# Optimization experiments

Hardware: AMD Instinct MI355X
Metric: run time of the kernel (lower is better)

The kernel has to match this reference:

```python
import jax, jax.numpy as jnp
import numpy as np

LN_EPS = 1e-5

def setup_inputs() -> dict:
    key = jax.random.key(0)
    ks = jax.random.split(key, 4)
    B, T, N, D, G = 8, 48, 1024, 64, 256
    x = jax.random.normal(ks[0], (B, T, N, D), dtype=jnp.float32)
    view = jax.random.uniform(ks[1], (G, N), dtype=jnp.float32)
    w = jax.random.normal(ks[2], (N, D, D), dtype=jnp.float32) * 0.02
    b = jax.random.normal(ks[3], (1, N, D), dtype=jnp.float32) * 0.02
    gamma = jnp.ones((D,), dtype=jnp.float32)
    beta = jnp.zeros((D,), dtype=jnp.float32)
    return {"x": x, "view": view, "w": w, "b": b, "gamma": gamma, "beta": beta}

def _layernorm(x, gamma, beta):
    mu = jnp.mean(x, axis=-1, keepdims=True)
    var = jnp.mean(jnp.square(x - mu), axis=-1, keepdims=True)
    return (x - mu) * jax.lax.rsqrt(var + LN_EPS) * gamma + beta

def reference(x, view, w, b, gamma, beta):
    # per-node linear transform: [B,T,N,D] x [N,D,D] -> [B,T,N,D]
    h = jnp.einsum('btni,nio->btno', x, w)
    h = h + b[0]  # bias broadcast over batch and time
    # grid aggregation via view mapping: [B,T,N,D] x [G,N] -> [B,T,G,D]
    g = jnp.einsum('btnd,gn->btgd', h, view)
    return _layernorm(g, gamma, beta)
```

## Files before the change

### kernel.cpp

```cpp
#include <hip/hip_runtime.h>
#include <stdint.h>
#include <stddef.h>


#define LNEPS 1e-5f

typedef __attribute__((ext_vector_type(8))) short bf16x8;
typedef __attribute__((ext_vector_type(4))) float f32x4;
typedef union { unsigned u[4]; bf16x8 v; } fragu;

static __device__ __forceinline__ unsigned rne(unsigned u) {
    return u + 0x7FFFu + ((u >> 16) & 1u);
}
static __device__ __forceinline__ void split_pair(float a, float b,
                                                  unsigned& hw_, unsigned& lw_) {
    unsigned ra = rne(__float_as_uint(a));
    unsigned rb = rne(__float_as_uint(b));
    hw_ = (ra >> 16) | (rb & 0xFFFF0000u);
    float fa = a - __uint_as_float(ra & 0xFFFF0000u);
    float fb = b - __uint_as_float(rb & 0xFFFF0000u);
    unsigned sa = rne(__float_as_uint(fa));
    unsigned sb = rne(__float_as_uint(fb));
    lw_ = (sa >> 16) | (sb & 0xFFFF0000u);
}
static __device__ __forceinline__ unsigned packhl(float vv) {
    unsigned r = rne(__float_as_uint(vv));
    unsigned hif = r & 0xFFFF0000u;
    float res = vv - __uint_as_float(hif);
    unsigned s = rne(__float_as_uint(res));
    return hif | (s >> 16);
}

static __device__ __forceinline__ void gll16(const void* g, void* l) {
    __builtin_amdgcn_global_load_lds(
        (const __attribute__((address_space(1))) void*)g,
        (__attribute__((address_space(3))) void*)l, 16, 0, 0);
}

#define WS_H   0u
#define WS_VH  100663296u
#define WS_VL  101187584u
#define WS_VB  101711872u

__global__ __launch_bounds__(256) void k0_prep(
        const float* __restrict__ view, const float* __restrict__ bias,
        unsigned short* __restrict__ vh, unsigned short* __restrict__ vl,
        float* __restrict__ vb) {
    const int g = blockIdx.x;
    const int tid = threadIdx.x;
    float4 vv = *(const float4*)(view + g * 1024 + tid * 4);
    unsigned h01, l01, h23, l23;
    split_pair(vv.x, vv.y, h01, l01);
    split_pair(vv.z, vv.w, h23, l23);
    *(uint2*)(vh + g * 1024 + tid * 4) = make_uint2(h01, h23);
    *(uint2*)(vl + g * 1024 + tid * 4) = make_uint2(l01, l23);
    const int q = tid >> 6, d = tid & 63;
    const float* vrow = view + g * 1024;
    float a = 0.f;
    #pragma unroll 8
    for (int nn = q * 256; nn < q * 256 + 256; ++nn)
        a = fmaf(vrow[nn], bias[nn * 64 + d], a);
    __shared__ float red[4][64];
    red[q][d] = a;
    __syncthreads();
    if (tid < 64)
        vb[g * 64 + tid] = red[0][tid] + red[1][tid] + red[2][tid] + red[3][tid];
}

__global__ __launch_bounds__(1024, 4) void k1_node(
        const float* __restrict__ x, const float* __restrict__ w,
        unsigned char* __restrict__ hb) {
    __shared__ float xs[16 * 16 * 64];
    __shared__ unsigned T[16 * 16 * 68];
    const int tid = threadIdx.x;
    const int l  = tid & 63, wv = tid >> 6;
    const int lc = l & 15,  lg = l >> 4;
    const int ng = blockIdx.x & 63, btg = blockIdx.x >> 6;
    const int n0 = ng * 16;
    const int bt_base = btg * 96;
    const int n = n0 + wv;

    bf16x8 bh[4][2], bl[4][2];
    #pragma unroll
    for (int cs = 0; cs < 4; ++cs) {
        #pragma unroll
        for (int kc = 0; kc < 2; ++kc) {
            const float* wp = w + (size_t)n * 4096 + (size_t)(kc * 32 + lg * 8) * 64
                                + cs * 16 + lc;
            float e[8];
            #pragma unroll
            for (int j = 0; j < 8; ++j) e[j] = wp[(size_t)j * 64];
            fragu H, L;
            #pragma unroll
            for (int k2 = 0; k2 < 4; ++k2)
                split_pair(e[2 * k2], e[2 * k2 + 1], H.u[k2], L.u[k2]);
            bh[cs][kc] = H.v;
            bl[cs][kc] = L.v;
        }
    }

#define K1_STAGE(T_) do {                                                     \
    _Pragma("unroll")                                                         \
    for (int c_ = 0; c_ < 4; ++c_) {                                          \
        int u_ = c_ * 1024 + tid;                                             \
        int btl_ = u_ >> 8, r_ = u_ & 255;                                    \
        int nn_ = r_ >> 4, q_ = r_ & 15;                                      \
        int ibp_ = q_ >> 1, hf_ = q_ & 1;                                     \
        int ibg_ = ibp_ ^ (btl_ & 7);                                         \
        const unsigned char* src_ = (const unsigned char*)x                   \
            + (size_t)(bt_base + (T_) * 16 + btl_) * 262144u                  \
            + (size_t)(n0 + nn_) * 256u + ibg_ * 32 + hf_ * 16;               \
        gll16(src_, (unsigned char*)xs + c_ * 16384 + wv * 1024);             \
    }                                                                         \
} while (0)

    K1_STAGE(0);
    for (int t = 0; t < 6; ++t) {
        __syncthreads();
        float4 xq[4];
        #pragma unroll
        for (int kc = 0; kc < 2; ++kc) {
            int ibp = (kc * 4 + lg) ^ (lc & 7);
            const float* rp = xs + lc * 1024 + wv * 64 + ibp * 8;
            xq[kc * 2]     = *(const float4*)(rp);
            xq[kc * 2 + 1] = *(const float4*)(rp + 4);
        }
        __syncthreads();
        if (t < 5) K1_STAGE(t + 1);

        bf16x8 ah[2], al[2];
        #pragma unroll
        for (int kc = 0; kc < 2; ++kc) {
            fragu H, L;
            split_pair(xq[kc * 2].x,     xq[kc * 2].y,     H.u[0], L.u[0]);
            split_pair(xq[kc * 2].z,     xq[kc * 2].w,     H.u[1], L.u[1]);
            split_pair(xq[kc * 2 + 1].x, xq[kc * 2 + 1].y, H.u[2], L.u[2]);
            split_pair(xq[kc * 2 + 1].z, xq[kc * 2 + 1].w, H.u[3], L.u[3]);
            ah[kc] = H.v;
            al[kc] = L.v;
        }
        f32x4 acc[4];
        #pragma unroll
        for (int cs = 0; cs < 4; ++cs) acc[cs] = (f32x4){0.f, 0.f, 0.f, 0.f};
        #pragma unroll
        for (int cs = 0; cs < 4; ++cs) {
            #pragma unroll
            for (int kc = 0; kc < 2; ++kc) {
                acc[cs] = __builtin_amdgcn_mfma_f32_16x16x32_bf16(ah[kc], bh[cs][kc], acc[cs], 0, 0, 0);
                acc[cs] = __builtin_amdgcn_mfma_f32_16x16x32_bf16(ah[kc], bl[cs][kc], acc[cs], 0, 0, 0);
                acc[cs] = __builtin_amdgcn_mfma_f32_16x16x32_bf16(al[kc], bh[cs][kc], acc[cs], 0, 0, 0);
                acc[cs] = __builtin_amdgcn_mfma_f32_16x16x32_bf16(al[kc], bl[cs][kc], acc[cs], 0, 0, 0);
            }
        }
        #pragma unroll
        for (int cs = 0; cs < 4; ++cs) {
            #pragma unroll
            for (int j = 0; j < 4; ++j)
                T[wv * 1088 + (lg * 4 + j) * 68 + cs * 16 + lc] = packhl(acc[cs][j]);
        }
        __syncthreads();
        {
            int btl = tid >> 6, d = tid & 63;
            unsigned vv[16];
            #pragma unroll
            for (int nn = 0; nn < 16; ++nn) vv[nn] = T[nn * 1088 + btl * 68 + d];
            unsigned hd[8], ld[8];
            #pragma unroll
            for (int k = 0; k < 8; ++k) {
                hd[k] = (vv[2 * k] >> 16) | (vv[2 * k + 1] & 0xFFFF0000u);
                ld[k] = (vv[2 * k] & 0xFFFFu) | (vv[2 * k + 1] << 16);
            }
            unsigned char* dst = hb + (size_t)(bt_base + t * 16 + btl) * 262144u
                                    + (size_t)d * 4096u + ng * 64;
            ((uint4*)dst)[0] = make_uint4(hd[0], hd[1], hd[2], hd[3]);
            ((uint4*)dst)[1] = make_uint4(hd[4], hd[5], hd[6], hd[7]);
            ((uint4*)dst)[2] = make_uint4(ld[0], ld[1], ld[2], ld[3]);
            ((uint4*)dst)[3] = make_uint4(ld[4], ld[5], ld[6], ld[7]);
        }
    }
#undef K1_STAGE
}

#define KB2 24576

__global__ __launch_bounds__(256, 3) void k2_grid(
        const unsigned short* __restrict__ vh, const unsigned short* __restrict__ vl,
        const unsigned char* __restrict__ hb, const float* __restrict__ vb,
        const float* __restrict__ gamma, const float* __restrict__ beta,
        float* __restrict__ out) {
    __shared__ __align__(16) unsigned char smem[2 * KB2];
    const int tid = threadIdx.x;
    const int l  = tid & 63;
    const int wv = tid >> 6;
    const int b  = blockIdx.x;
    const int bm = (b >> 3) & 1;
    const int bt = (b & 7) + (b >> 4) * 8;
    const int lc = l & 15, lg = l >> 4;

    const unsigned short* a_src[4];
    int a_dst[4];
    #pragma unroll
    for (int c = 0; c < 4; ++c) {
        int id = (wv * 4 + c) * 64 + l;
        int row = id >> 3;
        int slot = id & 7;
        int sg = slot ^ (row & 7);
        int plg = sg >> 2, kcg = sg & 3;
        const unsigned short* pl = plg ? vl : vh;
        a_src[c] = pl + (size_t)(bm * 128 + row) * 1024 + kcg * 8;
        a_dst[c] = (wv * 4 + c) * 1024;
    }
    const unsigned char* b_src[2];
    int b_dst[2];
    #pragma unroll
    for (int c = 0; c < 2; ++c) {
        int id = (wv * 2 + c) * 64 + l;
        int d_ = id >> 3;
        int slot = id & 7;
        int sg = slot ^ (d_ & 7);
        b_src[c] = hb + (size_t)bt * 262144u + (size_t)d_ * 4096u
                      + (sg >> 2) * 64 + ((sg >> 1) & 1) * 32 + (sg & 1) * 16;
        b_dst[c] = 16384 + (wv * 2 + c) * 1024;
    }
    int aoff[2][2];
    #pragma unroll
    for (int st = 0; st < 2; ++st)
        #pragma unroll
        for (int pl = 0; pl < 2; ++pl) {
            int row = wv * 32 + st * 16 + lc;
            aoff[st][pl] = row * 128 + ((((pl << 2) | lg) ^ (row & 7)) * 16);
        }
    int boff[4][2];
    #pragma unroll
    for (int cs = 0; cs < 4; ++cs)
        #pragma unroll
        for (int pl = 0; pl < 2; ++pl) {
            int d_ = cs * 16 + lc;
            int sg = ((lg >> 1) << 2) | (pl << 1) | (lg & 1);
            boff[cs][pl] = 16384 + d_ * 128 + ((sg ^ (d_ & 7)) * 16);
        }

    f32x4 acc[2][4];
    #pragma unroll
    for (int st = 0; st < 2; ++st)
        #pragma unroll
        for (int cs = 0; cs < 4; ++cs)
            acc[st][cs] = (f32x4){0.f, 0.f, 0.f, 0.f};

#define K2_STAGE(KB, S) do {                                                  \
    _Pragma("unroll")                                                         \
    for (int c_ = 0; c_ < 4; ++c_)                                            \
        gll16(a_src[c_] + (size_t)(S) * 32, smem + (KB) + a_dst[c_]);         \
    _Pragma("unroll")                                                         \
    for (int c_ = 0; c_ < 2; ++c_)                                            \
        gll16(b_src[c_] + (size_t)(S) * 128, smem + (KB) + b_dst[c_]);        \
} while (0)

    K2_STAGE(0, 0);
    __syncthreads();
    int kb = 0;
    for (int s = 0; s < 32; ++s) {
        if (s + 1 < 32) K2_STAGE(kb ^ KB2, s + 1);
        bf16x8 a0h = *(const bf16x8*)(smem + kb + aoff[0][0]);
        bf16x8 a0l = *(const bf16x8*)(smem + kb + aoff[0][1]);
        bf16x8 a1h = *(const bf16x8*)(smem + kb + aoff[1][0]);
        bf16x8 a1l = *(const bf16x8*)(smem + kb + aoff[1][1]);
        #pragma unroll
        for (int cs = 0; cs < 4; ++cs) {
            bf16x8 bhf = *(const bf16x8*)(smem + kb + boff[cs][0]);
            bf16x8 blf = *(const bf16x8*)(smem + kb + boff[cs][1]);
            acc[0][cs] = __builtin_amdgcn_mfma_f32_16x16x32_bf16(a0h, bhf, acc[0][cs], 0, 0, 0);
            acc[0][cs] = __builtin_amdgcn_mfma_f32_16x16x32_bf16(a0h, blf, acc[0][cs], 0, 0, 0);
            acc[0][cs] = __builtin_amdgcn_mfma_f32_16x16x32_bf16(a0l, bhf, acc[0][cs], 0, 0, 0);
            acc[1][cs] = __builtin_amdgcn_mfma_f32_16x16x32_bf16(a1h, bhf, acc[1][cs], 0, 0, 0);
            acc[1][cs] = __builtin_amdgcn_mfma_f32_16x16x32_bf16(a1h, blf, acc[1][cs], 0, 0, 0);
            acc[1][cs] = __builtin_amdgcn_mfma_f32_16x16x32_bf16(a1l, bhf, acc[1][cs], 0, 0, 0);
        }
        __syncthreads();
        kb ^= KB2;
    }

    float gam[4], bet[4];
    #pragma unroll
    for (int cs = 0; cs < 4; ++cs) {
        gam[cs] = gamma[cs * 16 + lc];
        bet[cs] = beta[cs * 16 + lc];
    }
    #pragma unroll
    for (int st = 0; st < 2; ++st) {
        #pragma unroll
        for (int j = 0; j < 4; ++j) {
            int g = bm * 128 + wv * 32 + st * 16 + lg * 4 + j;
            float v[4];
            float s1 = 0.f, s2 = 0.f;
            #pragma unroll
            for (int cs = 0; cs < 4; ++cs) {
                v[cs] = acc[st][cs][j] + vb[g * 64 + cs * 16 + lc];
                s1 += v[cs];
                s2 += v[cs] * v[cs];
            }
            s1 += __shfl_xor(s1, 1);  s2 += __shfl_xor(s2, 1);
            s1 += __shfl_xor(s1, 2);  s2 += __shfl_xor(s2, 2);
            s1 += __shfl_xor(s1, 4);  s2 += __shfl_xor(s2, 4);
            s1 += __shfl_xor(s1, 8);  s2 += __shfl_xor(s2, 8);
            float mu  = s1 * 0.015625f;
            float var = s2 * 0.015625f - mu * mu;
            float inv = rsqrtf(var + LNEPS);
            size_t ob = (size_t)bt * 16384u + (size_t)g * 64u;
            #pragma unroll
            for (int cs = 0; cs < 4; ++cs)
                out[ob + cs * 16 + lc] = (v[cs] - mu) * inv * gam[cs] + bet[cs];
        }
    }
#undef K2_STAGE
}

extern "C" void kernel_launch(void* const* d_in, const int* in_sizes, int n_in,
                              void* d_out, int out_size, void* d_ws, size_t ws_size,
                              hipStream_t stream) {
    (void)in_sizes; (void)n_in; (void)out_size; (void)ws_size;
    const float* x     = (const float*)d_in[0];
    const float* view  = (const float*)d_in[1];
    const float* w     = (const float*)d_in[2];
    const float* bias  = (const float*)d_in[3];
    const float* gamma = (const float*)d_in[4];
    const float* beta  = (const float*)d_in[5];
    float* out = (float*)d_out;

    char* ws = (char*)d_ws;
    unsigned char* hb  = (unsigned char*)(ws + WS_H);
    unsigned short* vh = (unsigned short*)(ws + WS_VH);
    unsigned short* vl = (unsigned short*)(ws + WS_VL);
    float* vb          = (float*)(ws + WS_VB);

    hipLaunchKernelGGL(k0_prep, dim3(256), dim3(256), 0, stream,
                       view, bias, vh, vl, vb);
    hipLaunchKernelGGL(k1_node, dim3(256), dim3(1024), 0, stream, x, w, hb);
    hipLaunchKernelGGL(k2_grid, dim3(768), dim3(256), 0, stream,
                       vh, vl, hb, vb, gamma, beta, out);
}
```

Baseline: 270.1 us.

## Load x directly into registers in k1 and use fine-grained waitcnt barriers in k2

In the node-transform kernel, the LDS staging of x through async global-to-LDS loads and its double barrier are removed. Each wave now reads its x fragments straight from global memory into registers, which frees the xs shared buffer and drops the minimum-blocks launch bound. In the grid kernel, __syncthreads is replaced by an explicit s_waitcnt vmcnt(6) plus s_barrier, so the prefetch of the next stage can stay in flight while the current stage is consumed. This trades the previous load overlap in k1 for less LDS traffic and synchronisation, and it relies on hand-counted outstanding-load counts being correct.

```diff
diff --git a/kernel.cpp b/kernel.cpp
--- a/kernel.cpp
+++ b/kernel.cpp
@@ -67,17 +67,15 @@
         vb[g * 64 + tid] = red[0][tid] + red[1][tid] + red[2][tid] + red[3][tid];
 }
 
-__global__ __launch_bounds__(1024, 4) void k1_node(
+__global__ __launch_bounds__(1024) void k1_node(
         const float* __restrict__ x, const float* __restrict__ w,
         unsigned char* __restrict__ hb) {
-    __shared__ float xs[16 * 16 * 64];
     __shared__ unsigned T[16 * 16 * 68];
     const int tid = threadIdx.x;
     const int l  = tid & 63, wv = tid >> 6;
     const int lc = l & 15,  lg = l >> 4;
     const int ng = blockIdx.x & 63, btg = blockIdx.x >> 6;
-    const int n0 = ng * 16;
-    const int bt_base = btg * 96;
+    const int n0 = ng * 16, bt_base = btg * 96;
     const int n = n0 + wv;
 
     bf16x8 bh[4][2], bl[4][2];
@@ -99,46 +97,35 @@
         }
     }
 
-#define K1_STAGE(T_) do {                                                     \
-    _Pragma("unroll")                                                         \
-    for (int c_ = 0; c_ < 4; ++c_) {                                          \
-        int u_ = c_ * 1024 + tid;                                             \
-        int btl_ = u_ >> 8, r_ = u_ & 255;                                    \
-        int nn_ = r_ >> 4, q_ = r_ & 15;                                      \
-        int ibp_ = q_ >> 1, hf_ = q_ & 1;                                     \
-        int ibg_ = ibp_ ^ (btl_ & 7);                                         \
-        const unsigned char* src_ = (const unsigned char*)x                   \
-            + (size_t)(bt_base + (T_) * 16 + btl_) * 262144u                  \
-            + (size_t)(n0 + nn_) * 256u + ibg_ * 32 + hf_ * 16;               \
-        gll16(src_, (unsigned char*)xs + c_ * 16384 + wv * 1024);             \
-    }                                                                         \
-} while (0)
-
-    K1_STAGE(0);
+    const int btl = tid >> 6;
+    const int dT  = tid & 63;
+
     for (int t = 0; t < 6; ++t) {
-        __syncthreads();
-        float4 xq[4];
-        #pragma unroll
-        for (int kc = 0; kc < 2; ++kc) {
-            int ibp = (kc * 4 + lg) ^ (lc & 7);
-            const float* rp = xs + lc * 1024 + wv * 64 + ibp * 8;
-            xq[kc * 2]     = *(const float4*)(rp);
-            xq[kc * 2 + 1] = *(const float4*)(rp + 4);
-        }
-        __syncthreads();
-        if (t < 5) K1_STAGE(t + 1);
+        const float* xp = x + (size_t)(bt_base + t * 16 + lc) * 65536u
+                            + (size_t)n * 64 + lg * 8;
+        float4 x0 = *(const float4*)(xp);
+        float4 x1 = *(const float4*)(xp + 4);
+        float4 x2 = *(const float4*)(xp + 32);
+        float4 x3 = *(const float4*)(xp + 36);
 
         bf16x8 ah[2], al[2];
-        #pragma unroll
-        for (int kc = 0; kc < 2; ++kc) {
+        {
             fragu H, L;
-            split_pair(xq[kc * 2].x,     xq[kc * 2].y,     H.u[0], L.u[0]);
-            split_pair(xq[kc * 2].z,     xq[kc * 2].w,     H.u[1], L.u[1]);
-            split_pair(xq[kc * 2 + 1].x, xq[kc * 2 + 1].y, H.u[2], L.u[2]);
-            split_pair(xq[kc * 2 + 1].z, xq[kc * 2 + 1].w, H.u[3], L.u[3]);
-            ah[kc] = H.v;
-            al[kc] = L.v;
-        }
+            split_pair(x0.x, x0.y, H.u[0], L.u[0]);
+            split_pair(x0.z, x0.w, H.u[1], L.u[1]);
+            split_pair(x1.x, x1.y, H.u[2], L.u[2]);
+            split_pair(x1.z, x1.w, H.u[3], L.u[3]);
+            ah[0] = H.v; al[0] = L.v;
+        }
+        {
+            fragu H, L;
+            split_pair(x2.x, x2.y, H.u[0], L.u[0]);
+            split_pair(x2.z, x2.w, H.u[1], L.u[1]);
+            split_pair(x3.x, x3.y, H.u[2], L.u[2]);
+            split_pair(x3.z, x3.w, H.u[3], L.u[3]);
+            ah[1] = H.v; al[1] = L.v;
+        }
+
         f32x4 acc[4];
         #pragma unroll
         for (int cs = 0; cs < 4; ++cs) acc[cs] = (f32x4){0.f, 0.f, 0.f, 0.f};
@@ -158,12 +145,13 @@
             for (int j = 0; j < 4; ++j)
                 T[wv * 1088 + (lg * 4 + j) * 68 + cs * 16 + lc] = packhl(acc[cs][j]);
         }
-        __syncthreads();
+        asm volatile("s_waitcnt lgkmcnt(0)" ::: "memory");
+        __builtin_amdgcn_s_barrier();
+
         {
-            int btl = tid >> 6, d = tid & 63;
             unsigned vv[16];
             #pragma unroll
-            for (int nn = 0; nn < 16; ++nn) vv[nn] = T[nn * 1088 + btl * 68 + d];
+            for (int nn = 0; nn < 16; ++nn) vv[nn] = T[nn * 1088 + btl * 68 + dT];
             unsigned hd[8], ld[8];
             #pragma unroll
             for (int k = 0; k < 8; ++k) {
@@ -171,14 +159,15 @@
                 ld[k] = (vv[2 * k] & 0xFFFFu) | (vv[2 * k + 1] << 16);
             }
             unsigned char* dst = hb + (size_t)(bt_base + t * 16 + btl) * 262144u
-                                    + (size_t)d * 4096u + ng * 64;
+                                    + (size_t)dT * 4096u + ng * 64;
             ((uint4*)dst)[0] = make_uint4(hd[0], hd[1], hd[2], hd[3]);
             ((uint4*)dst)[1] = make_uint4(hd[4], hd[5], hd[6], hd[7]);
             ((uint4*)dst)[2] = make_uint4(ld[0], ld[1], ld[2], ld[3]);
             ((uint4*)dst)[3] = make_uint4(ld[4], ld[5], ld[6], ld[7]);
         }
-    }
-#undef K1_STAGE
+        asm volatile("s_waitcnt lgkmcnt(0)" ::: "memory");
+        __builtin_amdgcn_s_barrier();
+    }
 }
 
 #define KB2 24576
@@ -257,10 +246,15 @@
 } while (0)
 
     K2_STAGE(0, 0);
-    __syncthreads();
     int kb = 0;
     for (int s = 0; s < 32; ++s) {
-        if (s + 1 < 32) K2_STAGE(kb ^ KB2, s + 1);
+        if (s < 31) {
+            K2_STAGE(kb ^ KB2, s + 1);
+            asm volatile("s_waitcnt vmcnt(6)" ::: "memory");
+        } else {
+            asm volatile("s_waitcnt vmcnt(0)" ::: "memory");
+        }
+        __builtin_amdgcn_s_barrier();
         bf16x8 a0h = *(const bf16x8*)(smem + kb + aoff[0][0]);
         bf16x8 a0l = *(const bf16x8*)(smem + kb + aoff[0][1]);
         bf16x8 a1h = *(const bf16x8*)(smem + kb + aoff[1][0]);
@@ -276,7 +270,7 @@
             acc[1][cs] = __builtin_amdgcn_mfma_f32_16x16x32_bf16(a1h, blf, acc[1][cs], 0, 0, 0);
             acc[1][cs] = __builtin_amdgcn_mfma_f32_16x16x32_bf16(a1l, bhf, acc[1][cs], 0, 0, 0);
         }
-        __syncthreads();
+        __builtin_amdgcn_s_barrier();
         kb ^= KB2;
     }
 
```

Result: no change. 271.9 us (+0.7%).
